# Kernel optimization log

Measured on AMD Instinct MI355X. Metric: run time of the kernel, lower is better.

Reference implementation:

```python
import jax, jax.numpy as jnp
import numpy as np

V = 50000   # num_candidates
D = 32      # dim_item
B = 4096    # batch
N = 16      # max_n_node
L = 20      # max_session_length
STEPS = 1   # propagation_steps


def setup_inputs() -> dict:
    key = jax.random.key(0)
    ks = jax.random.split(key, 19)
    s = 1.0 / np.sqrt(D)
    u = lambda k, shp: jax.random.uniform(k, shp, jnp.float32, -s, s)
    return {
        "alias_inputs": jax.random.randint(ks[0], (B, L), 0, N),
        "A": jax.random.uniform(ks[1], (B, N, 2 * N), jnp.float32),
        "items": jax.random.randint(ks[2], (B, N), 0, V),
        "mask": jnp.ones((B, L), jnp.int32),
        "emb": u(ks[3], (V, D)),
        "w_ih": u(ks[4], (3 * D, 2 * D)),
        "w_hh": u(ks[5], (3 * D, D)),
        "b_ih": u(ks[6], (3 * D,)),
        "b_hh": u(ks[7], (3 * D,)),
        "b_iah": u(ks[8], (D,)),
        "b_oah": u(ks[9], (D,)),
        "w_ein": u(ks[10], (D, D)),
        "b_ein": u(ks[11], (D,)),
        "w_eout": u(ks[12], (D, D)),
        "b_eout": u(ks[13], (D,)),
        "w1": u(ks[14], (D, D)),
        "b1": u(ks[15], (D,)),
        "w2": u(ks[16], (D, D)),
        "b2": u(ks[17], (D,)),
        "w3": u(ks[18], (D, 1)),
    }


def reference(alias_inputs, A, items, mask, emb, w_ih, w_hh, b_ih, b_hh,
              b_iah, b_oah, w_ein, b_ein, w_eout, b_eout, w1, b1, w2, b2, w3):
    # item embedding lookup: [B, N, D]
    h = emb[items]
    n = A.shape[1]
    for _ in range(STEPS):
        node_in = h @ w_ein + b_ein
        node_out = h @ w_eout + b_eout
        # adjacency message passing (incoming / outgoing halves of A)
        input_in = jnp.matmul(A[:, :, :n], node_in) + b_iah
        input_out = jnp.matmul(A[:, :, n:2 * n], node_out) + b_oah
        inputs = jnp.concatenate([input_in, input_out], axis=-1)  # [B,N,2D]
        gi = inputs @ w_ih.T + b_ih   # [B,N,3D]
        gh = h @ w_hh.T + b_hh        # [B,N,3D]
        i_r, i_i, i_n = jnp.split(gi, 3, axis=-1)
        h_r, h_i, h_n = jnp.split(gh, 3, axis=-1)
        resetgate = jax.nn.sigmoid(i_r + h_r)
        inputgate = jax.nn.sigmoid(i_i + h_i)
        newgate = jnp.tanh(i_n + resetgate * h_n)
        h = newgate + inputgate * (h - newgate)
    # per-sample gather: seq_hidden[b, t] = h[b, alias_inputs[b, t]]
    seq = jnp.take_along_axis(h, alias_inputs[:, :, None], axis=1)  # [B,L,D]
    last = jnp.sum(mask, axis=1) - 1
    ht = seq[jnp.arange(seq.shape[0]), last]  # [B,D]
    q1 = (ht @ w1 + b1)[:, None, :]           # [B,1,D]
    q2 = seq @ w2 + b2                        # [B,L,D]
    alpha = jax.nn.sigmoid(q1 + q2) @ w3      # [B,L,1]
    s_g = jnp.sum(alpha * seq * mask[:, :, None].astype(seq.dtype), axis=1)
    scores = s_g @ emb[1:].T                  # [B, V-1]
    return scores
```

## Files before the change

kernel.cpp:

```cpp
#include <hip/hip_runtime.h>
#include <hip/hip_bf16.h>


#define B_BATCH 4096
#define N_NODE  16
#define L_SEQ   20
#define D_DIM   32
#define NV_OUT  49999
#define EMB_ROWS 50176

typedef float  f32x4  __attribute__((ext_vector_type(4)));
typedef float  f32x4u __attribute__((ext_vector_type(4), aligned(4)));
typedef __bf16 bf16x8 __attribute__((ext_vector_type(8)));

__device__ __forceinline__ float sigf(float x) {
    return 1.0f / (1.0f + __expf(-x));
}

__global__ __launch_bounds__(256) void session3_kernel(
    const int*   __restrict__ alias_inputs,
    const float* __restrict__ A,
    const int*   __restrict__ items,
    const int*   __restrict__ mask,
    const float* __restrict__ emb,
    const float* __restrict__ w_ih,
    const float* __restrict__ w_hh,
    const float* __restrict__ b_ih, const float* __restrict__ b_hh,
    const float* __restrict__ b_iah, const float* __restrict__ b_oah,
    const float* __restrict__ w_ein, const float* __restrict__ b_ein,
    const float* __restrict__ w_eout, const float* __restrict__ b_eout,
    const float* __restrict__ w1, const float* __restrict__ b1,
    const float* __restrict__ w2, const float* __restrict__ b2,
    const float* __restrict__ w3,
    float* __restrict__ sg_out)
{
    const int b   = blockIdx.x;
    const int tid = threadIdx.x;
    const int g   = tid >> 5;
    const int d   = tid & 31;
    const int n0  = g, n1 = g + 8;

    __shared__ float h_s [N_NODE][D_DIM];
    __shared__ float A_s [N_NODE][2 * N_NODE];
    __shared__ float ni_s[N_NODE][D_DIM];
    __shared__ float no_s[N_NODE][D_DIM];
    __shared__ float ii_s[N_NODE][D_DIM];
    __shared__ float io_s[N_NODE][D_DIM];
    __shared__ float wih_s[96][66];
    __shared__ float whh_s[96][34];
    __shared__ float q1_s[D_DIM];
    __shared__ float alpha_s[L_SEQ];
    __shared__ int   last_s;

    for (int idx = tid; idx < 512; idx += 256) {
        const int n = idx >> 5, dd = idx & 31;
        const int it = items[b * N_NODE + n];
        h_s[n][dd] = emb[(size_t)it * D_DIM + dd];
        A_s[n][dd] = A[(size_t)b * 512 + idx];
    }
    for (int f = tid; f < 96 * 64; f += 256) wih_s[f >> 6][f & 63] = w_ih[f];
    for (int f = tid; f < 96 * 32; f += 256) whh_s[f >> 5][f & 31] = w_hh[f];
    __syncthreads();

    float ai0 = b_ein[d], ao0 = b_eout[d];
    float ai1 = ai0,      ao1 = ao0;
    #pragma unroll
    for (int kb = 0; kb < 8; ++kb) {
        const int k0 = kb * 4;
        const f32x4 h0v = *reinterpret_cast<const f32x4*>(&h_s[n0][k0]);
        const f32x4 h1v = *reinterpret_cast<const f32x4*>(&h_s[n1][k0]);
        #pragma unroll
        for (int j = 0; j < 4; ++j) {
            const int k = k0 + j;
            const float we = w_ein[k * 32 + d], wo = w_eout[k * 32 + d];
            ai0 += h0v[j] * we; ai1 += h1v[j] * we;
            ao0 += h0v[j] * wo; ao1 += h1v[j] * wo;
        }
    }
    ni_s[n0][d] = ai0; ni_s[n1][d] = ai1;
    no_s[n0][d] = ao0; no_s[n1][d] = ao1;
    __syncthreads();

    float iv0 = b_iah[d], ov0 = b_oah[d];
    float iv1 = iv0,      ov1 = ov0;
    #pragma unroll
    for (int mb = 0; mb < 4; ++mb) {
        const int m0 = mb * 4;
        const f32x4 a0i = *reinterpret_cast<const f32x4*>(&A_s[n0][m0]);
        const f32x4 a1i = *reinterpret_cast<const f32x4*>(&A_s[n1][m0]);
        const f32x4 a0o = *reinterpret_cast<const f32x4*>(&A_s[n0][N_NODE + m0]);
        const f32x4 a1o = *reinterpret_cast<const f32x4*>(&A_s[n1][N_NODE + m0]);
        #pragma unroll
        for (int j = 0; j < 4; ++j) {
            const int m = m0 + j;
            const float nim = ni_s[m][d], nom = no_s[m][d];
            iv0 += a0i[j] * nim;
            iv1 += a1i[j] * nim;
            ov0 += a0o[j] * nom;
            ov1 += a1o[j] * nom;
        }
    }
    ii_s[n0][d] = iv0; ii_s[n1][d] = iv1;
    io_s[n0][d] = ov0; io_s[n1][d] = ov1;
    __syncthreads();

    float r0 = b_ih[d] + b_hh[d],           r1 = r0;
    float i0 = b_ih[32 + d] + b_hh[32 + d], i1 = i0;
    float gn0 = b_ih[64 + d],               gn1 = gn0;
    float hn0 = b_hh[64 + d],               hn1 = hn0;
    #pragma unroll
    for (int kb = 0; kb < 8; ++kb) {
        const int k0 = kb * 4;
        const f32x4 a0v = *reinterpret_cast<const f32x4*>(&ii_s[n0][k0]);
        const f32x4 a1v = *reinterpret_cast<const f32x4*>(&ii_s[n1][k0]);
        const f32x4 o0v = *reinterpret_cast<const f32x4*>(&io_s[n0][k0]);
        const f32x4 o1v = *reinterpret_cast<const f32x4*>(&io_s[n1][k0]);
        const f32x4 h0v = *reinterpret_cast<const f32x4*>(&h_s[n0][k0]);
        const f32x4 h1v = *reinterpret_cast<const f32x4*>(&h_s[n1][k0]);
        #pragma unroll
        for (int j = 0; j < 4; ++j) {
            const int k = k0 + j;
            const float wri = wih_s[d][k],      wro = wih_s[d][32 + k];
            const float wii = wih_s[32 + d][k], wio = wih_s[32 + d][32 + k];
            const float wni = wih_s[64 + d][k], wno = wih_s[64 + d][32 + k];
            const float whr = whh_s[d][k];
            const float whi = whh_s[32 + d][k];
            const float whn = whh_s[64 + d][k];
            r0  += a0v[j] * wri + o0v[j] * wro + h0v[j] * whr;
            r1  += a1v[j] * wri + o1v[j] * wro + h1v[j] * whr;
            i0  += a0v[j] * wii + o0v[j] * wio + h0v[j] * whi;
            i1  += a1v[j] * wii + o1v[j] * wio + h1v[j] * whi;
            gn0 += a0v[j] * wni + o0v[j] * wno;
            gn1 += a1v[j] * wni + o1v[j] * wno;
            hn0 += h0v[j] * whn;
            hn1 += h1v[j] * whn;
        }
    }

    float hv0, hv1;
    {
        const float rg0 = sigf(r0), ig0 = sigf(i0);
        const float x0  = gn0 + rg0 * hn0;
        const float e0  = __expf(2.0f * fabsf(x0));
        const float ng0 = copysignf(1.0f - 2.0f / (e0 + 1.0f), x0);
        hv0 = ng0 + ig0 * (h_s[n0][d] - ng0);
        const float rg1 = sigf(r1), ig1 = sigf(i1);
        const float x1  = gn1 + rg1 * hn1;
        const float e1  = __expf(2.0f * fabsf(x1));
        const float ng1 = copysignf(1.0f - 2.0f / (e1 + 1.0f), x1);
        hv1 = ng1 + ig1 * (h_s[n1][d] - ng1);
    }
    __syncthreads();
    h_s[n0][d] = hv0;
    h_s[n1][d] = hv1;
    __syncthreads();

    for (int idx = tid; idx < L_SEQ * D_DIM; idx += 256) {
        const int t = idx >> 5, dd = idx & 31;
        const int a = alias_inputs[b * L_SEQ + t];
        const float v = h_s[a][dd];
        if (t < 16) ni_s[t][dd] = v;
        else        no_s[t - 16][dd] = v;
    }
    if (tid == 0) {
        int s = 0;
        for (int t = 0; t < L_SEQ; ++t) s += mask[b * L_SEQ + t];
        last_s = s - 1;
    }
    __syncthreads();

    if (tid < D_DIM) {
        const int lt = last_s;
        const float* sl = (lt < 16) ? &ni_s[lt][0] : &no_s[lt - 16][0];
        float acc = b1[tid];
        #pragma unroll
        for (int k = 0; k < 32; ++k) acc += sl[k] * w1[k * 32 + tid];
        q1_s[tid] = acc;
    }
    __syncthreads();

    for (int idx = tid; idx < L_SEQ * D_DIM; idx += 256) {
        const int t = idx >> 5, dd = idx & 31;
        const float* sp = (t < 16) ? &ni_s[t][0] : &no_s[t - 16][0];
        float q2 = b2[dd];
        #pragma unroll
        for (int k = 0; k < 32; ++k) q2 += sp[k] * w2[k * 32 + dd];
        const float val = sigf(q1_s[dd] + q2) * w3[dd];
        if (t < 16) ii_s[t][dd] = val;
        else        io_s[t - 16][dd] = val;
    }
    __syncthreads();
    if (tid < L_SEQ) {
        const float* tp = (tid < 16) ? &ii_s[tid][0] : &io_s[tid - 16][0];
        float a = 0.0f;
        #pragma unroll
        for (int dd = 0; dd < 32; ++dd) a += tp[dd];
        alpha_s[tid] = a * (float)mask[b * L_SEQ + tid];
    }
    __syncthreads();

    if (tid < D_DIM) {
        float acc = 0.0f;
        #pragma unroll
        for (int t = 0; t < L_SEQ; ++t) {
            const float sv = (t < 16) ? ni_s[t][tid] : no_s[t - 16][tid];
            acc += alpha_s[t] * sv;
        }
        sg_out[b * D_DIM + tid] = acc;
    }
}

__global__ __launch_bounds__(256) void conv_emb_kernel(
    const float* __restrict__ emb, __hip_bfloat16* __restrict__ emb_b)
{
    const int total = EMB_ROWS * D_DIM;
    for (int i = blockIdx.x * 256 + threadIdx.x; i < total; i += gridDim.x * 256) {
        const int v = i >> 5, k = i & 31;
        int src = v + 1;
        if (src > NV_OUT) src = NV_OUT;
        emb_b[i] = __float2bfloat16(emb[(size_t)src * D_DIM + k]);
    }
}

__global__ __launch_bounds__(256) void conv_sg_kernel(
    const float* __restrict__ sg,
    __hip_bfloat16* __restrict__ hi, __hip_bfloat16* __restrict__ lo)
{
    const int i = blockIdx.x * 256 + threadIdx.x;
    const float x = sg[i];
    const __hip_bfloat16 h = __float2bfloat16(x);
    hi[i] = h;
    lo[i] = __float2bfloat16(x - __bfloat162float(h));
}

__global__ __launch_bounds__(256) void score9_kernel(
    const __hip_bfloat16* __restrict__ sg_hi,
    const __hip_bfloat16* __restrict__ sg_lo,
    const __hip_bfloat16* __restrict__ emb_b,
    float* __restrict__ out)
{
    __shared__ float T[32][260];
    const int wave = threadIdx.x >> 6;
    const int lane = threadIdx.x & 63;
    const int rc   = lane & 15;
    const int kgrp = lane >> 4;
    const int b0   = blockIdx.y * 32;
    const int v0   = blockIdx.x * 256;
    const int vw   = v0 + wave * 64;

    const bf16x8 ah0 = *reinterpret_cast<const bf16x8*>(
        &sg_hi[(size_t)(b0 + rc) * D_DIM + kgrp * 8]);
    const bf16x8 al0 = *reinterpret_cast<const bf16x8*>(
        &sg_lo[(size_t)(b0 + rc) * D_DIM + kgrp * 8]);
    const bf16x8 ah1 = *reinterpret_cast<const bf16x8*>(
        &sg_hi[(size_t)(b0 + 16 + rc) * D_DIM + kgrp * 8]);
    const bf16x8 al1 = *reinterpret_cast<const bf16x8*>(
        &sg_lo[(size_t)(b0 + 16 + rc) * D_DIM + kgrp * 8]);

    #pragma unroll
    for (int s = 0; s < 4; ++s) {
        const int vt = vw + s * 16;
        const bf16x8 bf = *reinterpret_cast<const bf16x8*>(
            &emb_b[(size_t)(vt + rc) * D_DIM + kgrp * 8]);
        f32x4 acc0 = {0.0f, 0.0f, 0.0f, 0.0f};
        acc0 = __builtin_amdgcn_mfma_f32_16x16x32_bf16(ah0, bf, acc0, 0, 0, 0);
        acc0 = __builtin_amdgcn_mfma_f32_16x16x32_bf16(al0, bf, acc0, 0, 0, 0);
        f32x4 acc1 = {0.0f, 0.0f, 0.0f, 0.0f};
        acc1 = __builtin_amdgcn_mfma_f32_16x16x32_bf16(ah1, bf, acc1, 0, 0, 0);
        acc1 = __builtin_amdgcn_mfma_f32_16x16x32_bf16(al1, bf, acc1, 0, 0, 0);
        const int col = wave * 64 + s * 16 + rc;
        #pragma unroll
        for (int j = 0; j < 4; ++j) {
            T[kgrp * 4 + j][col]      = acc0[j];
            T[16 + kgrp * 4 + j][col] = acc1[j];
        }
    }
    __syncthreads();

    if (v0 + 256 <= NV_OUT) {
        #pragma unroll
        for (int r = 0; r < 8; ++r) {
            const int row = wave * 8 + r;
            const f32x4 val = *reinterpret_cast<const f32x4*>(&T[row][lane * 4]);
            *reinterpret_cast<f32x4u*>(
                &out[(size_t)(b0 + row) * NV_OUT + v0 + lane * 4]) = val;
        }
    } else {
        #pragma unroll
        for (int r = 0; r < 8; ++r) {
            const int row = wave * 8 + r;
            float* op = &out[(size_t)(b0 + row) * NV_OUT];
            #pragma unroll
            for (int j = 0; j < 4; ++j) {
                const int c = lane * 4 + j;
                if (v0 + c < NV_OUT) op[v0 + c] = T[row][c];
            }
        }
    }
}

extern "C" void kernel_launch(void* const* d_in, const int* in_sizes, int n_in,
                              void* d_out, int out_size, void* d_ws, size_t ws_size,
                              hipStream_t stream)
{
    const int*   alias_inputs = (const int*)  d_in[0];
    const float* A      = (const float*)d_in[1];
    const int*   items  = (const int*)  d_in[2];
    const int*   mask   = (const int*)  d_in[3];
    const float* emb    = (const float*)d_in[4];
    const float* w_ih   = (const float*)d_in[5];
    const float* w_hh   = (const float*)d_in[6];
    const float* b_ih   = (const float*)d_in[7];
    const float* b_hh   = (const float*)d_in[8];
    const float* b_iah  = (const float*)d_in[9];
    const float* b_oah  = (const float*)d_in[10];
    const float* w_ein  = (const float*)d_in[11];
    const float* b_ein  = (const float*)d_in[12];
    const float* w_eout = (const float*)d_in[13];
    const float* b_eout = (const float*)d_in[14];
    const float* w1     = (const float*)d_in[15];
    const float* b1     = (const float*)d_in[16];
    const float* w2     = (const float*)d_in[17];
    const float* b2     = (const float*)d_in[18];
    const float* w3     = (const float*)d_in[19];

    float* sg = (float*)d_ws;
    __hip_bfloat16* sg_hi = (__hip_bfloat16*)((char*)d_ws + 512 * 1024);
    __hip_bfloat16* sg_lo = (__hip_bfloat16*)((char*)d_ws + 768 * 1024);
    __hip_bfloat16* emb_b = (__hip_bfloat16*)((char*)d_ws + 1024 * 1024);
    float* out = (float*)d_out;

    hipLaunchKernelGGL(conv_emb_kernel, dim3(2048), dim3(256), 0, stream,
                       emb, emb_b);

    hipLaunchKernelGGL(session3_kernel, dim3(B_BATCH), dim3(256), 0, stream,
                       alias_inputs, A, items, mask, emb,
                       w_ih, w_hh, b_ih, b_hh, b_iah, b_oah,
                       w_ein, b_ein, w_eout, b_eout,
                       w1, b1, w2, b2, w3, sg);

    hipLaunchKernelGGL(conv_sg_kernel, dim3(B_BATCH * D_DIM / 256), dim3(256),
                       0, stream, sg, sg_hi, sg_lo);

    hipLaunchKernelGGL(score9_kernel,
                       dim3((NV_OUT + 255) / 256, B_BATCH / 32),
                       dim3(256), 0, stream, sg_hi, sg_lo, emb_b, out);
}
```

Before: 333.1 us.

## Fuse sg bf16 split into session kernel, shrink score tile, nontemporal stores

Computes the hi/lo bf16 split of the session vector directly in the session kernel, removing the separate conversion launch and the fp32 round trip. The scoring kernel now handles 16 batch rows per block instead of 32, doubling grid size and halving shared memory per block. Output writes use nontemporal stores to reduce cache pollution on the large score matrix. The smaller tile doubles embedding tile reloads per output element.

New measurement: 313.2 us. 1.06x faster.

```diff
diff --git a/kernel.cpp b/kernel.cpp
--- a/kernel.cpp
+++ b/kernel.cpp
@@ -32,7 +32,8 @@
     const float* __restrict__ w1, const float* __restrict__ b1,
     const float* __restrict__ w2, const float* __restrict__ b2,
     const float* __restrict__ w3,
-    float* __restrict__ sg_out)
+    __hip_bfloat16* __restrict__ sg_hi,
+    __hip_bfloat16* __restrict__ sg_lo)
 {
     const int b   = blockIdx.x;
     const int tid = threadIdx.x;
@@ -206,7 +207,9 @@
             const float sv = (t < 16) ? ni_s[t][tid] : no_s[t - 16][tid];
             acc += alpha_s[t] * sv;
         }
-        sg_out[b * D_DIM + tid] = acc;
+        const __hip_bfloat16 h = __float2bfloat16(acc);
+        sg_hi[b * D_DIM + tid] = h;
+        sg_lo[b * D_DIM + tid] = __float2bfloat16(acc - __bfloat162float(h));
     }
 }
 
@@ -222,73 +225,54 @@
     }
 }
 
-__global__ __launch_bounds__(256) void conv_sg_kernel(
-    const float* __restrict__ sg,
-    __hip_bfloat16* __restrict__ hi, __hip_bfloat16* __restrict__ lo)
-{
-    const int i = blockIdx.x * 256 + threadIdx.x;
-    const float x = sg[i];
-    const __hip_bfloat16 h = __float2bfloat16(x);
-    hi[i] = h;
-    lo[i] = __float2bfloat16(x - __bfloat162float(h));
-}
-
-__global__ __launch_bounds__(256) void score9_kernel(
+__global__ __launch_bounds__(256) void score8_kernel(
     const __hip_bfloat16* __restrict__ sg_hi,
     const __hip_bfloat16* __restrict__ sg_lo,
     const __hip_bfloat16* __restrict__ emb_b,
     float* __restrict__ out)
 {
-    __shared__ float T[32][260];
+    __shared__ float T[16][260];
     const int wave = threadIdx.x >> 6;
     const int lane = threadIdx.x & 63;
     const int rc   = lane & 15;
     const int kgrp = lane >> 4;
-    const int b0   = blockIdx.y * 32;
+    const int b0   = blockIdx.y * 16;
     const int v0   = blockIdx.x * 256;
     const int vw   = v0 + wave * 64;
 
-    const bf16x8 ah0 = *reinterpret_cast<const bf16x8*>(
+    const bf16x8 ah = *reinterpret_cast<const bf16x8*>(
         &sg_hi[(size_t)(b0 + rc) * D_DIM + kgrp * 8]);
-    const bf16x8 al0 = *reinterpret_cast<const bf16x8*>(
+    const bf16x8 al = *reinterpret_cast<const bf16x8*>(
         &sg_lo[(size_t)(b0 + rc) * D_DIM + kgrp * 8]);
-    const bf16x8 ah1 = *reinterpret_cast<const bf16x8*>(
-        &sg_hi[(size_t)(b0 + 16 + rc) * D_DIM + kgrp * 8]);
-    const bf16x8 al1 = *reinterpret_cast<const bf16x8*>(
-        &sg_lo[(size_t)(b0 + 16 + rc) * D_DIM + kgrp * 8]);
 
     #pragma unroll
     for (int s = 0; s < 4; ++s) {
         const int vt = vw + s * 16;
         const bf16x8 bf = *reinterpret_cast<const bf16x8*>(
             &emb_b[(size_t)(vt + rc) * D_DIM + kgrp * 8]);
-        f32x4 acc0 = {0.0f, 0.0f, 0.0f, 0.0f};
-        acc0 = __builtin_amdgcn_mfma_f32_16x16x32_bf16(ah0, bf, acc0, 0, 0, 0);
-        acc0 = __builtin_amdgcn_mfma_f32_16x16x32_bf16(al0, bf, acc0, 0, 0, 0);
-        f32x4 acc1 = {0.0f, 0.0f, 0.0f, 0.0f};
-        acc1 = __builtin_amdgcn_mfma_f32_16x16x32_bf16(ah1, bf, acc1, 0, 0, 0);
-        acc1 = __builtin_amdgcn_mfma_f32_16x16x32_bf16(al1, bf, acc1, 0, 0, 0);
+        f32x4 acc = {0.0f, 0.0f, 0.0f, 0.0f};
+        acc = __builtin_amdgcn_mfma_f32_16x16x32_bf16(ah, bf, acc, 0, 0, 0);
+        acc = __builtin_amdgcn_mfma_f32_16x16x32_bf16(al, bf, acc, 0, 0, 0);
         const int col = wave * 64 + s * 16 + rc;
         #pragma unroll
-        for (int j = 0; j < 4; ++j) {
-            T[kgrp * 4 + j][col]      = acc0[j];
-            T[16 + kgrp * 4 + j][col] = acc1[j];
-        }
+        for (int j = 0; j < 4; ++j)
+            T[kgrp * 4 + j][col] = acc[j];
     }
     __syncthreads();
 
     if (v0 + 256 <= NV_OUT) {
         #pragma unroll
-        for (int r = 0; r < 8; ++r) {
-            const int row = wave * 8 + r;
+        for (int r = 0; r < 4; ++r) {
+            const int row = wave * 4 + r;
             const f32x4 val = *reinterpret_cast<const f32x4*>(&T[row][lane * 4]);
-            *reinterpret_cast<f32x4u*>(
-                &out[(size_t)(b0 + row) * NV_OUT + v0 + lane * 4]) = val;
+            f32x4u* op = reinterpret_cast<f32x4u*>(
+                &out[(size_t)(b0 + row) * NV_OUT + v0 + lane * 4]);
+            __builtin_nontemporal_store(val, op);
         }
     } else {
         #pragma unroll
-        for (int r = 0; r < 8; ++r) {
-            const int row = wave * 8 + r;
+        for (int r = 0; r < 4; ++r) {
+            const int row = wave * 4 + r;
             float* op = &out[(size_t)(b0 + row) * NV_OUT];
             #pragma unroll
             for (int j = 0; j < 4; ++j) {
@@ -324,7 +308,6 @@
     const float* b2     = (const float*)d_in[18];
     const float* w3     = (const float*)d_in[19];
 
-    float* sg = (float*)d_ws;
     __hip_bfloat16* sg_hi = (__hip_bfloat16*)((char*)d_ws + 512 * 1024);
     __hip_bfloat16* sg_lo = (__hip_bfloat16*)((char*)d_ws + 768 * 1024);
     __hip_bfloat16* emb_b = (__hip_bfloat16*)((char*)d_ws + 1024 * 1024);
@@ -337,12 +320,9 @@
                        alias_inputs, A, items, mask, emb,
                        w_ih, w_hh, b_ih, b_hh, b_iah, b_oah,
                        w_ein, b_ein, w_eout, b_eout,
-                       w1, b1, w2, b2, w3, sg);
-
-    hipLaunchKernelGGL(conv_sg_kernel, dim3(B_BATCH * D_DIM / 256), dim3(256),
-                       0, stream, sg, sg_hi, sg_lo);
-
-    hipLaunchKernelGGL(score9_kernel,
-                       dim3((NV_OUT + 255) / 256, B_BATCH / 32),
+                       w1, b1, w2, b2, w3, sg_hi, sg_lo);
+
+    hipLaunchKernelGGL(score8_kernel,
+                       dim3((NV_OUT + 255) / 256, B_BATCH / 16),
                        dim3(256), 0, stream, sg_hi, sg_lo, emb_b, out);
 }
```
